# Kernel optimization log

Hardware: AMD Instinct MI355X
Metric: run time of the kernel (lower is better)

The kernel has to match this reference:

```python
import jax, jax.numpy as jnp
import numpy as np

B, T, D, U = 128, 512, 128, 512


def setup_inputs() -> dict:
    key = jax.random.key(0)
    kx, kwx, kwh = jax.random.split(key, 3)
    x = jax.random.normal(kx, (B, T, D), dtype=jnp.float32)
    Wx = jax.random.normal(kwx, (D, U), dtype=jnp.float32) * (1.0 / np.sqrt(D))
    Wh = jax.random.normal(kwh, (U, U), dtype=jnp.float32) * (1.0 / np.sqrt(U))
    b = jnp.zeros((U,), dtype=jnp.float32)
    return {"x": x, "Wx": Wx, "Wh": Wh, "b": b}


def reference(x, Wx, Wh, b):
    # Elman RNN: h_t = tanh(x_t @ Wx + h_{t-1} @ Wh + b)
    # Faithful to MyRNN(return_sequences=True): TensorArray.stack() -> [T, B, U]
    h0 = jnp.zeros((x.shape[0], Wh.shape[0]), dtype=x.dtype)  # fallback zero initial state
    xs = jnp.swapaxes(x, 0, 1)  # [T, B, D] for scan over time

    def step(h, x_t):
        h_new = jnp.tanh(x_t @ Wx + h @ Wh + b)
        return h_new, h_new

    _, seq = jax.lax.scan(step, h0, xs)
    return seq  # [T, B, U]
```

## Files before the change

kernel.cpp:

```cpp
#include <hip/hip_runtime.h>
#include <stddef.h>
#include <stdint.h>


constexpr int B = 128;
constexpr int T = 512;
constexpr int D = 128;
constexpr int U = 512;

typedef _Float16 f16;
typedef _Float16 f16x2 __attribute__((ext_vector_type(2)));
typedef _Float16 f16x8 __attribute__((ext_vector_type(8)));
typedef __fp16   fp16x2 __attribute__((ext_vector_type(2)));
typedef float    f32x4 __attribute__((ext_vector_type(4)));
typedef unsigned int u32;

union U32H2 { u32 u; f16x2 h; fp16x2 p; };

static __device__ __forceinline__ u32 pk(float a, float b) {
    U32H2 c; c.p = __builtin_amdgcn_cvt_pkrtz(a, b); return c.u;
}

#if __has_builtin(__builtin_amdgcn_fdot2)
static __device__ __forceinline__ float fdot2(u32 a, u32 b, float c) {
    U32H2 x, y; x.u = a; y.u = b;
    return __builtin_amdgcn_fdot2(x.h, y.h, c, false);
}
#else
static __device__ __forceinline__ float fdot2(u32 a, u32 b, float c) {
    U32H2 x, y; x.u = a; y.u = b;
    return c + (float)x.h.x * (float)y.h.x + (float)x.h.y * (float)y.h.y;
}
#endif

static __device__ __forceinline__ float fast_tanh(float x) {
    float e = __expf(2.0f * x);
    return 1.0f - 2.0f * __builtin_amdgcn_rcpf(e + 1.0f);
}

__global__ __launch_bounds__(256) void pgemm_kernel(
    const float* __restrict__ x,
    const float* __restrict__ Wx,
    const float* __restrict__ bias,
    float* __restrict__ P)
{
    __shared__ u32 xs[128][66];
    __shared__ u32 ws[64][132];

    const int rb  = blockIdx.x;
    const int cb  = blockIdx.y;
    const int tid = threadIdx.x;
    const int tr  = tid >> 4;
    const int tcc = tid & 15;

    const float4* x4 = (const float4*)x;
#pragma unroll
    for (int l = 0; l < 16; ++l) {
        int idx = tid + l * 256;
        int r   = idx >> 5;
        int q   = idx & 31;
        int m   = rb * 128 + r;
        int b_  = m & 127;
        int t_  = m >> 7;
        float4 v = x4[((size_t)b_ * T + t_) * 32 + q];
        xs[r][2 * q]     = pk(v.x, v.y);
        xs[r][2 * q + 1] = pk(v.z, v.w);
    }
    const float4* W4 = (const float4*)Wx;
#pragma unroll
    for (int l = 0; l < 8; ++l) {
        int idx = tid + l * 256;
        int kp  = idx >> 5;
        int q   = idx & 31;
        float4 a = W4[(size_t)(2 * kp)     * 128 + cb * 32 + q];
        float4 c = W4[(size_t)(2 * kp + 1) * 128 + cb * 32 + q];
        uint4 w;
        w.x = pk(a.x, c.x); w.y = pk(a.y, c.y);
        w.z = pk(a.z, c.z); w.w = pk(a.w, c.w);
        *(uint4*)&ws[kp][4 * q] = w;
    }
    __syncthreads();

    float acc[8][8];
#pragma unroll
    for (int i = 0; i < 8; ++i)
#pragma unroll
        for (int j = 0; j < 8; ++j) acc[i][j] = 0.f;

#pragma unroll 2
    for (int kp = 0; kp < 64; ++kp) {
        u32 xv[8], wv[8];
#pragma unroll
        for (int i = 0; i < 8; ++i) xv[i] = xs[tr + 16 * i][kp];
#pragma unroll
        for (int j = 0; j < 8; ++j) wv[j] = ws[kp][tcc + 16 * j];
#pragma unroll
        for (int i = 0; i < 8; ++i)
#pragma unroll
            for (int j = 0; j < 8; ++j)
                acc[i][j] = fdot2(xv[i], wv[j], acc[i][j]);
    }

#pragma unroll
    for (int j = 0; j < 8; ++j) {
        int c    = cb * 128 + tcc + 16 * j;
        float bv = bias[c];
#pragma unroll
        for (int i = 0; i < 8; ++i) {
            int m = rb * 128 + tr + 16 * i;
            P[(size_t)m * U + c] = acc[i][j] + bv;
        }
    }
}

__global__ __launch_bounds__(512, 2) void rnn_kernel(
    const float* __restrict__ Wh,
    float* __restrict__ out)
{
    __shared__ __align__(16) u32 WL[32768];
    __shared__ __align__(16) u32 hbuf[2][256];

    const int tid = threadIdx.x;
    const int w   = tid >> 6;
    const int l   = tid & 63;
    const int lg  = l >> 4;
    const int lc  = l & 15;
    const int b   = blockIdx.x;

    f16x8 Wf[4][12];
#pragma unroll
    for (int ct = 0; ct < 4; ++ct) {
#pragma unroll
        for (int s = 0; s < 12; ++s) {
            const float* src = Wh + (size_t)(32 * s + 8 * lg) * U
                             + 64 * w + 16 * ct + lc;
            f16x8 f;
#pragma unroll
            for (int e = 0; e < 8; ++e) f[e] = (f16)src[(size_t)e * U];
            Wf[ct][s] = f;
        }
    }
#pragma unroll
    for (int ct = 0; ct < 4; ++ct)
#pragma unroll
        for (int s = 0; s < 12; ++s)
            asm("" : "+v"(Wf[ct][s]));

#pragma unroll
    for (int sr = 0; sr < 4; ++sr) {
#pragma unroll
        for (int ct = 0; ct < 4; ++ct) {
            const float* src = Wh + (size_t)(32 * (12 + sr) + 8 * lg) * U
                             + 64 * w + 16 * ct + lc;
            f16x8 f;
#pragma unroll
            for (int e = 0; e < 8; ++e) f[e] = (f16)src[(size_t)e * U];
            *(f16x8*)&WL[((w * 16 + sr * 4 + ct) * 64 + l) * 4] = f;
        }
    }

    if (tid < 256) { hbuf[0][tid] = 0u; hbuf[1][tid] = 0u; }
    __syncthreads();

    float* outb = out + (size_t)b * U;

    float pv0 = 0.f, pv1 = 0.f, pv2 = 0.f, pv3 = 0.f;
    if (l < 16) {
        pv0 = outb[64 * w + 0  + lc];
        pv1 = outb[64 * w + 16 + lc];
        pv2 = outb[64 * w + 32 + lc];
        pv3 = outb[64 * w + 48 + lc];
    }

    for (int t = 0; t < T; ++t) {
        const int par = t & 1;
        const f16* hb = (const f16*)hbuf[par];

        f32x4 acc0 = (f32x4)0.f, acc1 = (f32x4)0.f;
        f32x4 acc2 = (f32x4)0.f, acc3 = (f32x4)0.f;

#define ALOAD(s) (*(const f16x8*)&hb[32 * (s) + 8 * lg])
#define WLREAD(fi) (*(const f16x8*)&WL[((w * 16 + (fi)) * 64 + l) * 4])

#pragma unroll
        for (int g = 0; g < 4; ++g) {
            f16x8 b0 = WLREAD(4 * g + 0);
            f16x8 b1 = WLREAD(4 * g + 1);
            f16x8 b2 = WLREAD(4 * g + 2);
            f16x8 b3 = WLREAD(4 * g + 3);
#pragma unroll
            for (int s = 3 * g; s < 3 * g + 3; ++s) {
                f16x8 a = ALOAD(s);
                acc0 = __builtin_amdgcn_mfma_f32_16x16x32_f16(a, Wf[0][s], acc0, 0, 0, 0);
                acc1 = __builtin_amdgcn_mfma_f32_16x16x32_f16(a, Wf[1][s], acc1, 0, 0, 0);
                acc2 = __builtin_amdgcn_mfma_f32_16x16x32_f16(a, Wf[2][s], acc2, 0, 0, 0);
                acc3 = __builtin_amdgcn_mfma_f32_16x16x32_f16(a, Wf[3][s], acc3, 0, 0, 0);
            }
            f16x8 a = ALOAD(12 + g);
            acc0 = __builtin_amdgcn_mfma_f32_16x16x32_f16(a, b0, acc0, 0, 0, 0);
            acc1 = __builtin_amdgcn_mfma_f32_16x16x32_f16(a, b1, acc1, 0, 0, 0);
            acc2 = __builtin_amdgcn_mfma_f32_16x16x32_f16(a, b2, acc2, 0, 0, 0);
            acc3 = __builtin_amdgcn_mfma_f32_16x16x32_f16(a, b3, acc3, 0, 0, 0);
        }
#undef ALOAD
#undef WLREAD

        float nv0 = 0.f, nv1 = 0.f, nv2 = 0.f, nv3 = 0.f;
        if (l < 16) {
            float* prow = outb + (size_t)t * (B * U);
            const float* prown = outb + (size_t)((t + 1 < T) ? t + 1 : t) * (B * U);
            f16* hbn = (f16*)hbuf[par ^ 1];

            float h0 = fast_tanh(pv0 + acc0.x);
            float h1 = fast_tanh(pv1 + acc1.x);
            float h2 = fast_tanh(pv2 + acc2.x);
            float h3 = fast_tanh(pv3 + acc3.x);
            prow[64 * w + 0  + lc] = h0;
            prow[64 * w + 16 + lc] = h1;
            prow[64 * w + 32 + lc] = h2;
            prow[64 * w + 48 + lc] = h3;
            hbn[64 * w + 0  + lc] = (f16)h0;
            hbn[64 * w + 16 + lc] = (f16)h1;
            hbn[64 * w + 32 + lc] = (f16)h2;
            hbn[64 * w + 48 + lc] = (f16)h3;

            nv0 = prown[64 * w + 0  + lc];
            nv1 = prown[64 * w + 16 + lc];
            nv2 = prown[64 * w + 32 + lc];
            nv3 = prown[64 * w + 48 + lc];
        }

        __syncthreads();
        pv0 = nv0; pv1 = nv1; pv2 = nv2; pv3 = nv3;
    }
}

extern "C" void kernel_launch(void* const* d_in, const int* in_sizes, int n_in,
                              void* d_out, int out_size, void* d_ws, size_t ws_size,
                              hipStream_t stream)
{
    (void)d_ws; (void)ws_size; (void)in_sizes; (void)n_in; (void)out_size;
    const float* x    = (const float*)d_in[0];
    const float* Wx   = (const float*)d_in[1];
    const float* Wh   = (const float*)d_in[2];
    const float* bias = (const float*)d_in[3];
    float* out = (float*)d_out;

    pgemm_kernel<<<dim3((T * B) / 128, U / 128), 256, 0, stream>>>(x, Wx, bias, out);
    rnn_kernel<<<B, 512, 0, stream>>>(Wh, out);
}
```

Measured before the change: 836.5 us.

## Compute fourth column tile per wave with VALU fdot2 alongside MFMA in RNN step

Each wave now computes three 16-column tiles with MFMA and the fourth 16-column tile with scalar fdot2 dot products. Four lanes split the K dimension and are combined with two xor shuffles. More of Wh stays in registers (Wf0, Wf1, Wf2, plus the packed Wv), so less of it is read from LDS each step. The h buffer is padded per 128-element segment to ease bank conflicts on the new uint4 reads. The goal is to overlap VALU work with the MFMA chain and shorten the serial per-step critical path, at the cost of much higher register pressure and possible spills.

```diff
diff --git a/kernel.cpp b/kernel.cpp
--- a/kernel.cpp
+++ b/kernel.cpp
@@ -117,121 +117,131 @@
     const float* __restrict__ Wh,
     float* __restrict__ out)
 {
-    __shared__ __align__(16) u32 WL[32768];
-    __shared__ __align__(16) u32 hbuf[2][256];
+    __shared__ __align__(16) u32 WL[20480];
+    __shared__ __align__(16) u32 hbuf[2][272];
 
     const int tid = threadIdx.x;
     const int w   = tid >> 6;
     const int l   = tid & 63;
     const int lg  = l >> 4;
     const int lc  = l & 15;
+    const int q   = l & 3;
+    const int vcol= 48 + (l >> 2);
     const int b   = blockIdx.x;
-
-    f16x8 Wf[4][12];
-#pragma unroll
-    for (int ct = 0; ct < 4; ++ct) {
-#pragma unroll
-        for (int s = 0; s < 12; ++s) {
-            const float* src = Wh + (size_t)(32 * s + 8 * lg) * U
-                             + 64 * w + 16 * ct + lc;
-            f16x8 f;
-#pragma unroll
-            for (int e = 0; e < 8; ++e) f[e] = (f16)src[(size_t)e * U];
-            Wf[ct][s] = f;
-        }
-    }
-#pragma unroll
-    for (int ct = 0; ct < 4; ++ct)
-#pragma unroll
-        for (int s = 0; s < 12; ++s)
-            asm("" : "+v"(Wf[ct][s]));
-
-#pragma unroll
-    for (int sr = 0; sr < 4; ++sr) {
-#pragma unroll
-        for (int ct = 0; ct < 4; ++ct) {
-            const float* src = Wh + (size_t)(32 * (12 + sr) + 8 * lg) * U
-                             + 64 * w + 16 * ct + lc;
-            f16x8 f;
-#pragma unroll
-            for (int e = 0; e < 8; ++e) f[e] = (f16)src[(size_t)e * U];
-            *(f16x8*)&WL[((w * 16 + sr * 4 + ct) * 64 + l) * 4] = f;
-        }
-    }
-
-    if (tid < 256) { hbuf[0][tid] = 0u; hbuf[1][tid] = 0u; }
+    const int cb  = 64 * w;
+
+    f16x8 Wf0[16], Wf1[16], Wf2[6];
+#pragma unroll
+    for (int s = 0; s < 16; ++s) {
+        const float* s0 = Wh + (size_t)(32 * s + 8 * lg) * U + cb + lc;
+        f16x8 f0, f1;
+#pragma unroll
+        for (int e = 0; e < 8; ++e) {
+            f0[e] = (f16)s0[(size_t)e * U];
+            f1[e] = (f16)s0[(size_t)e * U + 16];
+        }
+        Wf0[s] = f0; Wf1[s] = f1;
+    }
+#pragma unroll
+    for (int s = 0; s < 6; ++s) {
+        const float* s0 = Wh + (size_t)(32 * s + 8 * lg) * U + cb + 32 + lc;
+        f16x8 f;
+#pragma unroll
+        for (int e = 0; e < 8; ++e) f[e] = (f16)s0[(size_t)e * U];
+        Wf2[s] = f;
+    }
+#pragma unroll
+    for (int s = 0; s < 16; ++s) { asm("" : "+v"(Wf0[s])); asm("" : "+v"(Wf1[s])); }
+#pragma unroll
+    for (int s = 0; s < 6; ++s)  { asm("" : "+v"(Wf2[s])); }
+
+    u32 Wv[64];
+    {
+        const float* c0 = Wh + (size_t)(q * 128) * U + cb + vcol;
+#pragma unroll
+        for (int j = 0; j < 64; ++j)
+            Wv[j] = pk(c0[(size_t)(2 * j) * U], c0[(size_t)(2 * j + 1) * U]);
+#pragma unroll
+        for (int j = 0; j < 64; ++j) asm("" : "+v"(Wv[j]));
+    }
+
+#pragma unroll
+    for (int sr = 0; sr < 10; ++sr) {
+        const float* s0 = Wh + (size_t)(32 * (6 + sr) + 8 * lg) * U + cb + 32 + lc;
+        f16x8 f;
+#pragma unroll
+        for (int e = 0; e < 8; ++e) f[e] = (f16)s0[(size_t)e * U];
+        *(f16x8*)&WL[((w * 10 + sr) * 64 + l) * 4] = f;
+    }
+
+    if (tid < 272) { hbuf[0][tid] = 0u; hbuf[1][tid] = 0u; }
     __syncthreads();
 
     float* outb = out + (size_t)b * U;
 
-    float pv0 = 0.f, pv1 = 0.f, pv2 = 0.f, pv3 = 0.f;
+    float pv0 = 0.f, pv1 = 0.f, pv2 = 0.f, pvv = 0.f;
     if (l < 16) {
-        pv0 = outb[64 * w + 0  + lc];
-        pv1 = outb[64 * w + 16 + lc];
-        pv2 = outb[64 * w + 32 + lc];
-        pv3 = outb[64 * w + 48 + lc];
-    }
+        pv0 = outb[cb + 0  + lc];
+        pv1 = outb[cb + 16 + lc];
+        pv2 = outb[cb + 32 + lc];
+    }
+    if (q == 0) pvv = outb[cb + vcol];
 
     for (int t = 0; t < T; ++t) {
         const int par = t & 1;
-        const f16* hb = (const f16*)hbuf[par];
-
-        f32x4 acc0 = (f32x4)0.f, acc1 = (f32x4)0.f;
-        f32x4 acc2 = (f32x4)0.f, acc3 = (f32x4)0.f;
-
-#define ALOAD(s) (*(const f16x8*)&hb[32 * (s) + 8 * lg])
-#define WLREAD(fi) (*(const f16x8*)&WL[((w * 16 + (fi)) * 64 + l) * 4])
-
-#pragma unroll
-        for (int g = 0; g < 4; ++g) {
-            f16x8 b0 = WLREAD(4 * g + 0);
-            f16x8 b1 = WLREAD(4 * g + 1);
-            f16x8 b2 = WLREAD(4 * g + 2);
-            f16x8 b3 = WLREAD(4 * g + 3);
-#pragma unroll
-            for (int s = 3 * g; s < 3 * g + 3; ++s) {
-                f16x8 a = ALOAD(s);
-                acc0 = __builtin_amdgcn_mfma_f32_16x16x32_f16(a, Wf[0][s], acc0, 0, 0, 0);
-                acc1 = __builtin_amdgcn_mfma_f32_16x16x32_f16(a, Wf[1][s], acc1, 0, 0, 0);
-                acc2 = __builtin_amdgcn_mfma_f32_16x16x32_f16(a, Wf[2][s], acc2, 0, 0, 0);
-                acc3 = __builtin_amdgcn_mfma_f32_16x16x32_f16(a, Wf[3][s], acc3, 0, 0, 0);
-            }
-            f16x8 a = ALOAD(12 + g);
-            acc0 = __builtin_amdgcn_mfma_f32_16x16x32_f16(a, b0, acc0, 0, 0, 0);
-            acc1 = __builtin_amdgcn_mfma_f32_16x16x32_f16(a, b1, acc1, 0, 0, 0);
+        const f16* hb  = (const f16*)hbuf[par];
+        const u32* hbu = hbuf[par];
+
+        f32x4 acc0 = (f32x4)0.f, acc1 = (f32x4)0.f, acc2 = (f32x4)0.f;
+        float accv = 0.f;
+
+#define ALOAD(s) (*(const f16x8*)&hb[((s) >> 2) * 136 + ((s) & 3) * 32 + 8 * lg])
+
+#pragma unroll
+        for (int s = 0; s < 16; ++s) {
+            uint4 hq = *(const uint4*)&hbu[q * 68 + 4 * s];
+            f16x8 a = ALOAD(s);
+            acc0 = __builtin_amdgcn_mfma_f32_16x16x32_f16(a, Wf0[s], acc0, 0, 0, 0);
+            acc1 = __builtin_amdgcn_mfma_f32_16x16x32_f16(a, Wf1[s], acc1, 0, 0, 0);
+            f16x8 b2 = (s < 6) ? Wf2[s]
+                     : *(const f16x8*)&WL[((w * 10 + (s - 6)) * 64 + l) * 4];
             acc2 = __builtin_amdgcn_mfma_f32_16x16x32_f16(a, b2, acc2, 0, 0, 0);
-            acc3 = __builtin_amdgcn_mfma_f32_16x16x32_f16(a, b3, acc3, 0, 0, 0);
+            accv = fdot2(hq.x, Wv[4 * s + 0], accv);
+            accv = fdot2(hq.y, Wv[4 * s + 1], accv);
+            accv = fdot2(hq.z, Wv[4 * s + 2], accv);
+            accv = fdot2(hq.w, Wv[4 * s + 3], accv);
         }
 #undef ALOAD
-#undef WLREAD
-
-        float nv0 = 0.f, nv1 = 0.f, nv2 = 0.f, nv3 = 0.f;
+
+        accv += __shfl_xor(accv, 1);
+        accv += __shfl_xor(accv, 2);
+
+        float* prow = outb + (size_t)t * (B * U);
+        const float* prown = outb + (size_t)((t + 1 < T) ? t + 1 : t) * (B * U);
+        f16* hbn = (f16*)hbuf[par ^ 1];
+
+        float nv0 = 0.f, nv1 = 0.f, nv2 = 0.f, nvv = 0.f;
         if (l < 16) {
-            float* prow = outb + (size_t)t * (B * U);
-            const float* prown = outb + (size_t)((t + 1 < T) ? t + 1 : t) * (B * U);
-            f16* hbn = (f16*)hbuf[par ^ 1];
-
             float h0 = fast_tanh(pv0 + acc0.x);
             float h1 = fast_tanh(pv1 + acc1.x);
             float h2 = fast_tanh(pv2 + acc2.x);
-            float h3 = fast_tanh(pv3 + acc3.x);
-            prow[64 * w + 0  + lc] = h0;
-            prow[64 * w + 16 + lc] = h1;
-            prow[64 * w + 32 + lc] = h2;
-            prow[64 * w + 48 + lc] = h3;
-            hbn[64 * w + 0  + lc] = (f16)h0;
-            hbn[64 * w + 16 + lc] = (f16)h1;
-            hbn[64 * w + 32 + lc] = (f16)h2;
-            hbn[64 * w + 48 + lc] = (f16)h3;
-
-            nv0 = prown[64 * w + 0  + lc];
-            nv1 = prown[64 * w + 16 + lc];
-            nv2 = prown[64 * w + 32 + lc];
-            nv3 = prown[64 * w + 48 + lc];
+            int c0 = cb + lc, c1 = cb + 16 + lc, c2 = cb + 32 + lc;
+            prow[c0] = h0; prow[c1] = h1; prow[c2] = h2;
+            hbn[(c0 >> 7) * 136 + (c0 & 127)] = (f16)h0;
+            hbn[(c1 >> 7) * 136 + (c1 & 127)] = (f16)h1;
+            hbn[(c2 >> 7) * 136 + (c2 & 127)] = (f16)h2;
+            nv0 = prown[c0]; nv1 = prown[c1]; nv2 = prown[c2];
+        }
+        if (q == 0) {
+            int c3 = cb + vcol;
+            float hv = fast_tanh(pvv + accv);
+            prow[c3] = hv;
+            hbn[(c3 >> 7) * 136 + (c3 & 127)] = (f16)hv;
+            nvv = prown[c3];
         }
 
         __syncthreads();
-        pv0 = nv0; pv1 = nv1; pv2 = nv2; pv3 = nv3;
+        pv0 = nv0; pv1 = nv1; pv2 = nv2; pvv = nvv;
     }
 }
 
```

Measured after the change: 1.205 ms. +44.0%, slower.
